# Optimization experiments

Measured on AMD Instinct MI355X. Metric: run time of the kernel, lower is better.

## Reference

```python
import jax, jax.numpy as jnp
import numpy as np

D = 1024
H = 16
HD = D // H
MLP = 4 * D
EPS = 1e-5


def layernorm(x, g, b):
    mu = jnp.mean(x, axis=-1, keepdims=True)
    var = jnp.mean(jnp.square(x - mu), axis=-1, keepdims=True)
    return (x - mu) * jax.lax.rsqrt(var + EPS) * g + b


def setup_inputs() -> dict:
    key = jax.random.key(0)
    ks = jax.random.split(key, 12)
    s = 0.02
    return {
        "x": jax.random.normal(ks[0], (2, 2048, D), jnp.float32),
        "ln1_g": jnp.ones((D,), jnp.float32),
        "ln1_b": jnp.zeros((D,), jnp.float32),
        "lnm_g": jnp.ones((D,), jnp.float32),
        "lnm_b": jnp.zeros((D,), jnp.float32),
        "qkv_w": jax.random.normal(ks[1], (D, 3 * D), jnp.float32) * s,
        "qkv_b": jnp.zeros((3 * D,), jnp.float32),
        "proj_w": jax.random.normal(ks[2], (D, D), jnp.float32) * s,
        "proj_b": jnp.zeros((D,), jnp.float32),
        "fc1_w": jax.random.normal(ks[3], (D, MLP), jnp.float32) * s,
        "fc1_b": jnp.zeros((MLP,), jnp.float32),
        "fc2_w": jax.random.normal(ks[4], (MLP, D), jnp.float32) * s,
        "fc2_b": jnp.zeros((D,), jnp.float32),
    }


def reference(x, ln1_g, ln1_b, lnm_g, lnm_b, qkv_w, qkv_b, proj_w, proj_b,
              fc1_w, fc1_b, fc2_w, fc2_b):
    B, N, _ = x.shape
    scale = HD ** -0.5
    # --- self-attention on norm1(x) ---
    h = layernorm(x, ln1_g, ln1_b)
    qkv = h @ qkv_w + qkv_b                       # [B, N, 3D]
    qkv = qkv.reshape(B, N, 3, H, HD)
    q, k, v = qkv[:, :, 0], qkv[:, :, 1], qkv[:, :, 2]  # [B, N, H, HD]
    attn = jnp.einsum("bqhd,bkhd->bhqk", q, k) * scale
    attn = jax.nn.softmax(attn, axis=-1)
    o = jnp.einsum("bhqk,bkhd->bqhd", attn, v).reshape(B, N, D)
    x = x + (o @ proj_w + proj_b)
    # --- MLP ---
    m = layernorm(x, lnm_g, lnm_b)
    m = jax.nn.gelu(m @ fc1_w + fc1_b, approximate=False)
    x = x + (m @ fc2_w + fc2_b)
    return x
```

## Files before the change

### kernel.cpp

```cpp
#include <hip/hip_runtime.h>

typedef __bf16 bf16_t;
typedef bf16_t bf16x8 __attribute__((ext_vector_type(8)));
typedef float f32x4 __attribute__((ext_vector_type(4)));
typedef unsigned short u16x8 __attribute__((ext_vector_type(8)));

#define MFMA(a, b, c) __builtin_amdgcn_mfma_f32_16x16x32_bf16(a, b, c, 0, 0, 0)

__device__ inline float exp2_fast(float x) {
  float r;
  asm volatile("v_exp_f32 %0, %1" : "=v"(r) : "v"(x));
  return r;
}

__device__ inline void gll16(const bf16_t* g, bf16_t* l) {
  __builtin_amdgcn_global_load_lds(
      (const __attribute__((address_space(1))) unsigned int*)(g),
      (__attribute__((address_space(3))) unsigned int*)(l), 16, 0, 0);
}

__global__ __launch_bounds__(256) void ln_kernel(const float* __restrict__ x,
                                                 const float* __restrict__ g,
                                                 const float* __restrict__ b,
                                                 bf16_t* __restrict__ out) {
  long row = blockIdx.x;
  const float4* xr = (const float4*)(x + row * 1024);
  float4 v = xr[threadIdx.x];
  float s = v.x + v.y + v.z + v.w;
  float s2 = v.x * v.x + v.y * v.y + v.z * v.z + v.w * v.w;
#pragma unroll
  for (int m = 32; m >= 1; m >>= 1) {
    s += __shfl_xor(s, m);
    s2 += __shfl_xor(s2, m);
  }
  __shared__ float red[8];
  int wid = threadIdx.x >> 6;
  if ((threadIdx.x & 63) == 0) {
    red[wid] = s;
    red[4 + wid] = s2;
  }
  __syncthreads();
  s = red[0] + red[1] + red[2] + red[3];
  s2 = red[4] + red[5] + red[6] + red[7];
  float mu = s * (1.f / 1024.f);
  float rs = rsqrtf(s2 * (1.f / 1024.f) - mu * mu + 1e-5f);
  float4 gv = ((const float4*)g)[threadIdx.x];
  float4 bv = ((const float4*)b)[threadIdx.x];
  bf16_t o0 = (bf16_t)((v.x - mu) * rs * gv.x + bv.x);
  bf16_t o1 = (bf16_t)((v.y - mu) * rs * gv.y + bv.y);
  bf16_t o2 = (bf16_t)((v.z - mu) * rs * gv.z + bv.z);
  bf16_t o3 = (bf16_t)((v.w - mu) * rs * gv.w + bv.w);
  ushort4 pk;
  pk.x = *(unsigned short*)&o0;
  pk.y = *(unsigned short*)&o1;
  pk.z = *(unsigned short*)&o2;
  pk.w = *(unsigned short*)&o3;
  *(ushort4*)(out + row * 1024 + threadIdx.x * 4) = pk;
}

__global__ void wconv_kernel(const float* __restrict__ W, bf16_t* __restrict__ Wt,
                             int K, int N) {
  __shared__ float t[32][33];
  int n0 = blockIdx.x * 32, k0 = blockIdx.y * 32;
#pragma unroll
  for (int s = 0; s < 4; s++) {
    int k = threadIdx.y + s * 8;
    t[k][threadIdx.x] = W[(long)(k0 + k) * N + n0 + threadIdx.x];
  }
  __syncthreads();
#pragma unroll
  for (int s = 0; s < 4; s++) {
    int n = threadIdx.y + s * 8;
    Wt[(long)(n0 + n) * K + k0 + threadIdx.x] = (bf16_t)t[threadIdx.x][n];
  }
}

#define BK 32

__global__ __launch_bounds__(256) void gemm_kernel(
    const bf16_t* __restrict__ A, const bf16_t* __restrict__ Bt,
    const float* __restrict__ bias, const float* __restrict__ resid,
    void* __restrict__ Cout, int M, int N, int K, int epi) {
  __shared__ bf16_t lA[128 * BK];
  __shared__ bf16_t lB[128 * BK];
  int tid = threadIdx.x;
  int bn = blockIdx.x, bm = blockIdx.y;
  int lane = tid & 63, w = tid >> 6;
  int quad = lane >> 4, l15 = lane & 15;
  int wm = (w & 1) * 64, wn = (w >> 1) * 64;

  f32x4 acc[4][4];
#pragma unroll
  for (int i = 0; i < 4; i++)
#pragma unroll
    for (int j = 0; j < 4; j++) acc[i][j] = (f32x4){0.f, 0.f, 0.f, 0.f};

  const bf16_t* ga = A + (long)(bm * 128 + w * 32 + (lane >> 2)) * K + (lane & 3) * 8;
  const bf16_t* gb = Bt + (long)(bn * 128 + w * 32 + (lane >> 2)) * K + (lane & 3) * 8;
  bf16_t* la = lA + w * 1024 + lane * 8;
  bf16_t* lb = lB + w * 1024 + lane * 8;
  long rowstep = (long)16 * K;

  for (int k0 = 0; k0 < K; k0 += BK) {
    __syncthreads();
    gll16(ga + k0, la);
    gll16(ga + k0 + rowstep, la + 512);
    gll16(gb + k0, lb);
    gll16(gb + k0 + rowstep, lb + 512);
    __syncthreads();
    bf16x8 af[4], bfr[4];
#pragma unroll
    for (int mt = 0; mt < 4; mt++)
      af[mt] = *(const bf16x8*)(lA + (wm + mt * 16 + l15) * BK + quad * 8);
#pragma unroll
    for (int nt = 0; nt < 4; nt++)
      bfr[nt] = *(const bf16x8*)(lB + (wn + nt * 16 + l15) * BK + quad * 8);
#pragma unroll
    for (int mt = 0; mt < 4; mt++)
#pragma unroll
      for (int nt = 0; nt < 4; nt++)
        acc[mt][nt] = MFMA(af[mt], bfr[nt], acc[mt][nt]);
  }

#pragma unroll
  for (int mt = 0; mt < 4; mt++) {
#pragma unroll
    for (int r = 0; r < 4; r++) {
      long row = bm * 128 + wm + mt * 16 + quad * 4 + r;
#pragma unroll
      for (int nt = 0; nt < 4; nt++) {
        int col = bn * 128 + wn + nt * 16 + l15;
        float v = acc[mt][nt][r] + bias[col];
        long idx = row * N + col;
        if (epi == 1) {
          ((float*)Cout)[idx] = v + resid[idx];
        } else if (epi == 2) {
          float gl = 0.5f * v * (1.0f + erff(v * 0.70710678118f));
          ((bf16_t*)Cout)[idx] = (bf16_t)gl;
        } else {
          ((bf16_t*)Cout)[idx] = (bf16_t)v;
        }
      }
    }
  }
}

#define LDV 72

__global__ __launch_bounds__(256) void attn_kernel(const bf16_t* __restrict__ qkv,
                                                   bf16_t* __restrict__ o) {
  const int LD = 3072;
  int flat = blockIdx.x;
  int slot = flat >> 3;
  int bh = (flat & 7) * 4 + (slot >> 5);
  int qt = slot & 31;
  int h = bh & 15, b = bh >> 4;

  int tid = threadIdx.x, w = tid >> 6, lane = tid & 63;
  int quad = lane >> 4, l15 = lane & 15;
  int qrow = qt * 64 + w * 16;
  const bf16_t* base = qkv + (long)b * 2048 * LD + h * 64;
  const bf16_t* Qp = base;
  const bf16_t* Kp = base + 1024;
  const bf16_t* Vp = base + 2048;

  __shared__ bf16_t lK[64 * 64];
  __shared__ bf16_t lV[64 * LDV];
  __shared__ bf16_t lP[4][16 * LDV];
  bf16_t* myp = lP[w];

  const bf16_t* kg =
      Kp + (long)(w * 16 + (lane >> 3)) * LD + (((lane & 7) ^ (lane >> 3)) & 7) * 8;
  bf16_t* lkd = lK + w * 1024 + lane * 8;
  int kk = tid & 31;
  int d0 = (tid >> 5) * 8;
  const bf16_t* vg = Vp + (long)(2 * kk) * LD + d0;
  unsigned int* lvw = (unsigned int*)lV;

  bf16x8 qf[2];
#pragma unroll
  for (int d = 0; d < 2; d++)
    qf[d] = *(const bf16x8*)(Qp + (long)(qrow + l15) * LD + d * 32 + quad * 8);

  f32x4 oacc[4];
#pragma unroll
  for (int t = 0; t < 4; t++) oacc[t] = (f32x4){0.f, 0.f, 0.f, 0.f};
  float li_p[4] = {0.f, 0.f, 0.f, 0.f};
  const float c2 = 0.18033688011112042f;

  int sw0 = (quad ^ l15) & 7;
  int sw1 = ((quad + 4) ^ l15) & 7;

  for (int kt = 0; kt < 2048; kt += 64) {
    long koff = (long)kt * LD;
    u16x8 va = *(const u16x8*)(vg + koff);
    u16x8 vb = *(const u16x8*)(vg + koff + LD);
    __syncthreads();
    gll16(kg + koff, lkd);
    gll16(kg + koff + 8 * (long)LD, lkd + 512);
#pragma unroll
    for (int j = 0; j < 8; j++)
      lvw[(d0 + j) * (LDV / 2) + kk] = (unsigned int)va[j] | ((unsigned int)vb[j] << 16);
    __syncthreads();

    f32x4 s[4];
#pragma unroll
    for (int st = 0; st < 4; st++) {
      const bf16_t* krow = lK + (st * 16 + l15) * 64;
      f32x4 z = (f32x4){0.f, 0.f, 0.f, 0.f};
      z = MFMA(qf[0], *(const bf16x8*)(krow + sw0 * 8), z);
      s[st] = MFMA(qf[1], *(const bf16x8*)(krow + sw1 * 8), z);
    }

#pragma unroll
    for (int st = 0; st < 4; st++)
#pragma unroll
      for (int r = 0; r < 4; r++) {
        float p = exp2_fast(s[st][r] * c2);
        s[st][r] = p;
        li_p[r] += p;
      }

#pragma unroll
    for (int r = 0; r < 4; r++)
#pragma unroll
      for (int st = 0; st < 4; st++)
        myp[(quad * 4 + r) * LDV + st * 16 + l15] = (bf16_t)s[st][r];
    asm volatile("s_waitcnt lgkmcnt(0)" ::: "memory");

    bf16x8 pa0 = *(const bf16x8*)(myp + l15 * LDV + quad * 8);
    bf16x8 pa1 = *(const bf16x8*)(myp + l15 * LDV + 32 + quad * 8);
#pragma unroll
    for (int t = 0; t < 4; t++) {
      const bf16_t* vr = lV + (t * 16 + l15) * LDV + quad * 8;
      oacc[t] = MFMA(pa0, *(const bf16x8*)(vr), oacc[t]);
      oacc[t] = MFMA(pa1, *(const bf16x8*)(vr + 32), oacc[t]);
    }
  }

  float li[4];
#pragma unroll
  for (int r = 0; r < 4; r++) {
    float s = li_p[r];
#pragma unroll
    for (int x = 8; x >= 1; x >>= 1) s += __shfl_xor(s, x);
    li[r] = s;
  }
#pragma unroll
  for (int t = 0; t < 4; t++)
#pragma unroll
    for (int r = 0; r < 4; r++) {
      long q = qrow + quad * 4 + r;
      o[((long)b * 2048 + q) * 1024 + h * 64 + t * 16 + l15] =
          (bf16_t)(oacc[t][r] / li[r]);
    }
}

extern "C" void kernel_launch(void* const* d_in, const int* in_sizes, int n_in,
                              void* d_out, int out_size, void* d_ws, size_t ws_size,
                              hipStream_t stream) {
  (void)in_sizes; (void)n_in; (void)out_size; (void)ws_size;
  const float* x = (const float*)d_in[0];
  const float* ln1_g = (const float*)d_in[1];
  const float* ln1_b = (const float*)d_in[2];
  const float* lnm_g = (const float*)d_in[3];
  const float* lnm_b = (const float*)d_in[4];
  const float* qkv_w = (const float*)d_in[5];
  const float* qkv_b = (const float*)d_in[6];
  const float* proj_w = (const float*)d_in[7];
  const float* proj_b = (const float*)d_in[8];
  const float* fc1_w = (const float*)d_in[9];
  const float* fc1_b = (const float*)d_in[10];
  const float* fc2_w = (const float*)d_in[11];
  const float* fc2_b = (const float*)d_in[12];
  float* out = (float*)d_out;

  const int M = 4096;
  const int D_ = 1024, MLP_ = 4096, QKV = 3072;

  char* ws = (char*)d_ws;
  bf16_t* h = (bf16_t*)(ws);
  bf16_t* qkvb = (bf16_t*)(ws + (8u << 20));
  bf16_t* ob = (bf16_t*)(ws + (32u << 20));
  float* x1 = (float*)(ws + (40u << 20));
  bf16_t* mb = (bf16_t*)(ws + (56u << 20));
  bf16_t* gb = (bf16_t*)(ws + (64u << 20));
  bf16_t* qkv_wt = (bf16_t*)(ws + (96u << 20));
  bf16_t* proj_wt = (bf16_t*)(ws + (102u << 20));
  bf16_t* fc1_wt = (bf16_t*)(ws + (104u << 20));
  bf16_t* fc2_wt = (bf16_t*)(ws + (112u << 20));

  dim3 tb(32, 8);
  wconv_kernel<<<dim3(QKV / 32, D_ / 32), tb, 0, stream>>>(qkv_w, qkv_wt, D_, QKV);
  wconv_kernel<<<dim3(D_ / 32, D_ / 32), tb, 0, stream>>>(proj_w, proj_wt, D_, D_);
  wconv_kernel<<<dim3(MLP_ / 32, D_ / 32), tb, 0, stream>>>(fc1_w, fc1_wt, D_, MLP_);
  wconv_kernel<<<dim3(D_ / 32, MLP_ / 32), tb, 0, stream>>>(fc2_w, fc2_wt, MLP_, D_);

  ln_kernel<<<M, 256, 0, stream>>>(x, ln1_g, ln1_b, h);
  gemm_kernel<<<dim3(QKV / 128, M / 128), 256, 0, stream>>>(h, qkv_wt, qkv_b, nullptr,
                                                            qkvb, M, QKV, D_, 0);
  attn_kernel<<<1024, 256, 0, stream>>>(qkvb, ob);
  gemm_kernel<<<dim3(D_ / 128, M / 128), 256, 0, stream>>>(ob, proj_wt, proj_b, x, x1,
                                                           M, D_, D_, 1);
  ln_kernel<<<M, 256, 0, stream>>>(x1, lnm_g, lnm_b, mb);
  gemm_kernel<<<dim3(MLP_ / 128, M / 128), 256, 0, stream>>>(mb, fc1_wt, fc1_b, nullptr,
                                                             gb, M, MLP_, D_, 2);
  gemm_kernel<<<dim3(D_ / 128, M / 128), 256, 0, stream>>>(gb, fc2_wt, fc2_b, x1, out,
                                                           M, D_, MLP_, 1);
}
```

Before: 467.0 us.

## Double-buffer GEMM LDS tiles, swizzle block order, split-K the fc2 GEMM

The GEMM now uses two LDS buffers so the async global-to-LDS load of the next K-slice is issued before the MFMAs on the current one. This hides load latency and halves the barriers per K step. Block indices are remapped in strides of eight, which changes which tiles run together and is meant to improve L2 reuse. The fc2 GEMM (K=4096, only 256 tiles) is split over two K-halves written as fp32 partials into reused workspace. A new elementwise kernel then adds the partials, bias and residual. That adds extra fp32 traffic and a launch in exchange for more parallelism.

```diff
diff --git a/kernel.cpp b/kernel.cpp
--- a/kernel.cpp
+++ b/kernel.cpp
@@ -75,16 +75,38 @@
   }
 }
 
-#define BK 32
+#define STAGE(BA, BB, k0)                                      \
+  gll16(ga + (k0), BA + w * 1024);                             \
+  gll16(ga + (k0) + rowstep, BA + w * 1024 + 512);             \
+  gll16(gb + (k0), BB + w * 1024);                             \
+  gll16(gb + (k0) + rowstep, BB + w * 1024 + 512);
+
+#define COMPUTE(LA, LB)                                                         \
+  {                                                                             \
+    bf16x8 af[4], bfr[4];                                                       \
+    _Pragma("unroll") for (int mt = 0; mt < 4; mt++) af[mt] =                   \
+        *(const bf16x8*)(LA + (wm + mt * 16 + l15) * 32 + quad * 8);            \
+    _Pragma("unroll") for (int nt = 0; nt < 4; nt++) bfr[nt] =                  \
+        *(const bf16x8*)(LB + (wn + nt * 16 + l15) * 32 + quad * 8);            \
+    _Pragma("unroll") for (int mt = 0; mt < 4; mt++)                            \
+        _Pragma("unroll") for (int nt = 0; nt < 4; nt++) acc[mt][nt] =          \
+            MFMA(af[mt], bfr[nt], acc[mt][nt]);                                 \
+  }
 
 __global__ __launch_bounds__(256) void gemm_kernel(
     const bf16_t* __restrict__ A, const bf16_t* __restrict__ Bt,
     const float* __restrict__ bias, const float* __restrict__ resid,
     void* __restrict__ Cout, int M, int N, int K, int epi) {
-  __shared__ bf16_t lA[128 * BK];
-  __shared__ bf16_t lB[128 * BK];
+  __shared__ bf16_t lA0[128 * 32], lB0[128 * 32];
+  __shared__ bf16_t lA1[128 * 32], lB1[128 * 32];
   int tid = threadIdx.x;
-  int bn = blockIdx.x, bm = blockIdx.y;
+  int nb = gridDim.x * gridDim.y;
+  int lin = blockIdx.y * gridDim.x + blockIdx.x;
+  int id = (lin & 7) * (nb >> 3) + (lin >> 3);
+  int bn = id % gridDim.x, bm = id / gridDim.x;
+  int kchunk = K / gridDim.z;
+  int kbeg = blockIdx.z * kchunk, kend = kbeg + kchunk;
+
   int lane = tid & 63, w = tid >> 6;
   int quad = lane >> 4, l15 = lane & 15;
   int wm = (w & 1) * 64, wn = (w >> 1) * 64;
@@ -97,29 +119,16 @@
 
   const bf16_t* ga = A + (long)(bm * 128 + w * 32 + (lane >> 2)) * K + (lane & 3) * 8;
   const bf16_t* gb = Bt + (long)(bn * 128 + w * 32 + (lane >> 2)) * K + (lane & 3) * 8;
-  bf16_t* la = lA + w * 1024 + lane * 8;
-  bf16_t* lb = lB + w * 1024 + lane * 8;
   long rowstep = (long)16 * K;
 
-  for (int k0 = 0; k0 < K; k0 += BK) {
+  STAGE(lA0, lB0, kbeg);
+  for (int k0 = kbeg; k0 < kend; k0 += 64) {
     __syncthreads();
-    gll16(ga + k0, la);
-    gll16(ga + k0 + rowstep, la + 512);
-    gll16(gb + k0, lb);
-    gll16(gb + k0 + rowstep, lb + 512);
+    STAGE(lA1, lB1, k0 + 32);
+    COMPUTE(lA0, lB0);
     __syncthreads();
-    bf16x8 af[4], bfr[4];
-#pragma unroll
-    for (int mt = 0; mt < 4; mt++)
-      af[mt] = *(const bf16x8*)(lA + (wm + mt * 16 + l15) * BK + quad * 8);
-#pragma unroll
-    for (int nt = 0; nt < 4; nt++)
-      bfr[nt] = *(const bf16x8*)(lB + (wn + nt * 16 + l15) * BK + quad * 8);
-#pragma unroll
-    for (int mt = 0; mt < 4; mt++)
-#pragma unroll
-      for (int nt = 0; nt < 4; nt++)
-        acc[mt][nt] = MFMA(af[mt], bfr[nt], acc[mt][nt]);
+    if (k0 + 64 < kend) { STAGE(lA0, lB0, k0 + 64); }
+    COMPUTE(lA1, lB1);
   }
 
 #pragma unroll
@@ -130,19 +139,41 @@
 #pragma unroll
       for (int nt = 0; nt < 4; nt++) {
         int col = bn * 128 + wn + nt * 16 + l15;
-        float v = acc[mt][nt][r] + bias[col];
         long idx = row * N + col;
-        if (epi == 1) {
-          ((float*)Cout)[idx] = v + resid[idx];
-        } else if (epi == 2) {
-          float gl = 0.5f * v * (1.0f + erff(v * 0.70710678118f));
-          ((bf16_t*)Cout)[idx] = (bf16_t)gl;
+        if (epi == 3) {
+          ((float*)Cout)[(long)blockIdx.z * M * N + idx] = acc[mt][nt][r];
         } else {
-          ((bf16_t*)Cout)[idx] = (bf16_t)v;
+          float v = acc[mt][nt][r] + bias[col];
+          if (epi == 1) {
+            ((float*)Cout)[idx] = v + resid[idx];
+          } else if (epi == 2) {
+            float gl = 0.5f * v * (1.0f + erff(v * 0.70710678118f));
+            ((bf16_t*)Cout)[idx] = (bf16_t)gl;
+          } else {
+            ((bf16_t*)Cout)[idx] = (bf16_t)v;
+          }
         }
       }
     }
   }
+}
+
+__global__ __launch_bounds__(256) void reduce2_kernel(const float* __restrict__ p0,
+                                                      const float* __restrict__ p1,
+                                                      const float* __restrict__ bias,
+                                                      const float* __restrict__ resid,
+                                                      float* __restrict__ out) {
+  long i = (long)blockIdx.x * 256 + threadIdx.x;
+  float4 a = ((const float4*)p0)[i];
+  float4 c = ((const float4*)p1)[i];
+  float4 r = ((const float4*)resid)[i];
+  float4 bv = ((const float4*)bias)[i & 255];
+  float4 o;
+  o.x = a.x + c.x + r.x + bv.x;
+  o.y = a.y + c.y + r.y + bv.y;
+  o.z = a.z + c.z + r.z + bv.z;
+  o.w = a.w + c.w + r.w + bv.w;
+  ((float4*)out)[i] = o;
 }
 
 #define LDV 72
@@ -171,7 +202,7 @@
 
   const bf16_t* kg =
       Kp + (long)(w * 16 + (lane >> 3)) * LD + (((lane & 7) ^ (lane >> 3)) & 7) * 8;
-  bf16_t* lkd = lK + w * 1024 + lane * 8;
+  bf16_t* lkd = lK + w * 1024;
   int kk = tid & 31;
   int d0 = (tid >> 5) * 8;
   const bf16_t* vg = Vp + (long)(2 * kk) * LD + d0;
@@ -289,6 +320,7 @@
   bf16_t* proj_wt = (bf16_t*)(ws + (102u << 20));
   bf16_t* fc1_wt = (bf16_t*)(ws + (104u << 20));
   bf16_t* fc2_wt = (bf16_t*)(ws + (112u << 20));
+  float* p01 = (float*)(ws);
 
   dim3 tb(32, 8);
   wconv_kernel<<<dim3(QKV / 32, D_ / 32), tb, 0, stream>>>(qkv_w, qkv_wt, D_, QKV);
@@ -305,6 +337,8 @@
   ln_kernel<<<M, 256, 0, stream>>>(x1, lnm_g, lnm_b, mb);
   gemm_kernel<<<dim3(MLP_ / 128, M / 128), 256, 0, stream>>>(mb, fc1_wt, fc1_b, nullptr,
                                                              gb, M, MLP_, D_, 2);
-  gemm_kernel<<<dim3(D_ / 128, M / 128), 256, 0, stream>>>(gb, fc2_wt, fc2_b, x1, out,
-                                                           M, D_, MLP_, 1);
-}
+  gemm_kernel<<<dim3(D_ / 128, M / 128, 2), 256, 0, stream>>>(gb, fc2_wt, nullptr,
+                                                              nullptr, p01, M, D_,
+                                                              MLP_, 3);
+  reduce2_kernel<<<4096, 256, 0, stream>>>(p01, p01 + (long)M * D_, fc2_b, x1, out);
+}
```

After: 459.8 us. Within noise of the previous version (-1.6%).
